# Kernel optimization log

Measured on AMD Instinct MI355X. Metric: run time of the kernel, lower is better.

Reference implementation:

```python
import jax, jax.numpy as jnp
import numpy as np

B, N, H = 1024, 4096, 32


def setup_inputs() -> dict:
    key = jax.random.key(0)
    ks = jax.random.split(key, 9)
    node_embedding = jax.random.normal(ks[0], (B, N, H), dtype=jnp.float32)
    mask = jax.random.randint(ks[1], (B, N), 0, 2).astype(jnp.float32)
    times = jax.random.uniform(ks[2], (B,), dtype=jnp.float32)
    idxc = jax.random.randint(ks[3], (B, 1), 0, N)
    # parameters
    vf = jax.random.uniform(ks[4], (1, H), dtype=jnp.float32)
    lim1 = 1.0 / np.sqrt(2 * H + 1)
    W1 = jax.random.uniform(ks[5], (H, 2 * H + 1), minval=-lim1, maxval=lim1, dtype=jnp.float32)
    b1 = jax.random.uniform(ks[6], (H,), minval=-lim1, maxval=lim1, dtype=jnp.float32)
    limh = 1.0 / np.sqrt(H)
    Wq = jax.random.uniform(ks[7], (H, H), minval=-limh, maxval=limh, dtype=jnp.float32)
    Wk = jax.random.uniform(ks[8], (H, H), minval=-limh, maxval=limh, dtype=jnp.float32)
    return {"node_embedding": node_embedding, "mask": mask, "times": times,
            "vf": vf, "W1": W1, "b1": b1, "Wq": Wq, "Wk": Wk, "idxc": idxc}


def reference(node_embedding, mask, times, vf, W1, b1, Wq, Wk, idxc):
    h = node_embedding.shape[-1]
    node_avg = jnp.mean(node_embedding, axis=1)                       # [B, H]
    # gather per-batch context node (idxc path; vf used only when idxc is None)
    f = jnp.take_along_axis(node_embedding, idxc[:, :, None], axis=1)[:, 0, :]  # [B, H]
    cat = jnp.concatenate([node_avg, f, times[:, None]], axis=1)      # [B, 2H+1]
    emb = cat @ W1.T + b1                                             # [B, H]
    q = emb @ Wq.T                                                    # [B, H]
    k = node_embedding @ Wk.T                                         # [B, N, H]
    scores = jnp.einsum('bh,bnh->bn', q, k) / jnp.sqrt(jnp.asarray(h, emb.dtype))
    scores = scores - mask * 999999999.0
    return jax.nn.softmax(scores, axis=-1)
```

## Files before the change

### kernel.cpp

```cpp
#include <hip/hip_runtime.h>
#include <math.h>

#define BB 1024
#define NN 4096
#define HH 32
#define PP 4
#define RK1 (NN / PP)

typedef float floatx4 __attribute__((ext_vector_type(4)));

#define WS_PART 0

__global__ __launch_bounds__(256) void k1_colsum(
    const float* __restrict__ ne, float* __restrict__ ws)
{
    const int blk = blockIdx.x;
    const int b   = blk >> 2;
    const int p   = blk & (PP - 1);
    const int tid = threadIdx.x;
    const int q8  = tid & 7;
    const int r   = tid >> 3;

    __shared__ float s_part[256 * 4];

    const float* base = ne + (size_t)b * (NN * HH)
                           + (size_t)(p * RK1 + r) * HH + q8 * 4;
    float a0 = 0.f, a1 = 0.f, a2 = 0.f, a3 = 0.f;
    #pragma unroll 8
    for (int i = 0; i < RK1 / 32; ++i) {
        const floatx4 v = __builtin_nontemporal_load(
            reinterpret_cast<const floatx4*>(base + i * (32 * HH)));
        a0 += v.x; a1 += v.y; a2 += v.z; a3 += v.w;
    }
    *reinterpret_cast<float4*>(&s_part[tid * 4]) = make_float4(a0, a1, a2, a3);
    __syncthreads();

    if (tid < HH) {
        const int q = tid >> 2, j = tid & 3;
        float s = 0.f;
        #pragma unroll
        for (int rr = 0; rr < 32; ++rr) s += s_part[(rr * 8 + q) * 4 + j];
        ws[WS_PART + (b * PP + p) * HH + tid] = s;
    }
}

__global__ __launch_bounds__(256) void k3_scores(
    const float* __restrict__ ne, const float* __restrict__ mask,
    const float* __restrict__ times,
    const float* __restrict__ W1, const float* __restrict__ b1,
    const float* __restrict__ Wq, const float* __restrict__ Wk,
    const int* __restrict__ idxc,
    const float* __restrict__ ws, float* __restrict__ out)
{
    const int b   = blockIdx.x;
    const int tid = threadIdx.x;
    const int q8  = tid & 7;
    const int r   = tid >> 3;

    __shared__ float s_scores[NN];
    __shared__ float sh_avg[HH], sh_f[HH], sh_emb[HH], sh_qk[HH];
    __shared__ float red_buf[4];

    if (tid < HH) {
        float s = 0.f;
        #pragma unroll
        for (int p = 0; p < PP; ++p) s += ws[WS_PART + (b * PP + p) * HH + tid];
        sh_avg[tid] = s * (1.0f / (float)NN);
        sh_f[tid]   = ne[(size_t)b * (NN * HH) + (size_t)idxc[b] * HH + tid];
    }
    __syncthreads();
    if (tid < HH) {
        const float t = times[b];
        const float* w = W1 + tid * (2 * HH + 1);
        float e = b1[tid];
        #pragma unroll
        for (int j = 0; j < HH; ++j) e += sh_avg[j] * w[j];
        #pragma unroll
        for (int j = 0; j < HH; ++j) e += sh_f[j] * w[HH + j];
        e += t * w[2 * HH];
        sh_emb[tid] = e;
    }
    __syncthreads();
    if (tid < HH) {
        const float* w = Wq + tid * HH;
        float qv = 0.f;
        #pragma unroll
        for (int j = 0; j < HH; ++j) qv += sh_emb[j] * w[j];
        sh_f[tid] = qv;
    }
    __syncthreads();
    if (tid < HH) {
        float s = 0.f;
        #pragma unroll
        for (int h = 0; h < HH; ++h) s += sh_f[h] * Wk[h * HH + tid];
        sh_qk[tid] = s * 0.17677669529663687f;
    }
    __syncthreads();

    const float kq0 = sh_qk[q8 * 4 + 0];
    const float kq1 = sh_qk[q8 * 4 + 1];
    const float kq2 = sh_qk[q8 * 4 + 2];
    const float kq3 = sh_qk[q8 * 4 + 3];

    const float* base = ne + (size_t)b * (NN * HH) + (size_t)r * HH + q8 * 4;

    #pragma unroll 8
    for (int i = 0; i < NN / 32; ++i) {
        const floatx4 v = __builtin_nontemporal_load(
            reinterpret_cast<const floatx4*>(base + i * (32 * HH)));
        float p = v.x * kq0 + v.y * kq1 + v.z * kq2 + v.w * kq3;
        p += __shfl_xor(p, 1);
        p += __shfl_xor(p, 2);
        p += __shfl_xor(p, 4);
        if (q8 == 0) s_scores[r + i * 32] = p;
    }
    __syncthreads();

    const float* mrow = mask + (size_t)b * NN;
    float lmax = -INFINITY;
    #pragma unroll
    for (int k = 0; k < NN / 1024; ++k) {
        const int n4 = tid + k * 256;
        const floatx4 mv = __builtin_nontemporal_load(
            reinterpret_cast<const floatx4*>(mrow + n4 * 4));
        float4 sv = *reinterpret_cast<const float4*>(&s_scores[n4 * 4]);
        sv.x -= mv.x * 999999999.0f;
        sv.y -= mv.y * 999999999.0f;
        sv.z -= mv.z * 999999999.0f;
        sv.w -= mv.w * 999999999.0f;
        *reinterpret_cast<float4*>(&s_scores[n4 * 4]) = sv;
        lmax = fmaxf(lmax, fmaxf(fmaxf(sv.x, sv.y), fmaxf(sv.z, sv.w)));
    }
    #pragma unroll
    for (int m = 1; m < 64; m <<= 1) lmax = fmaxf(lmax, __shfl_xor(lmax, m));
    if ((tid & 63) == 0) red_buf[tid >> 6] = lmax;
    __syncthreads();
    const float bmax = fmaxf(fmaxf(red_buf[0], red_buf[1]),
                             fmaxf(red_buf[2], red_buf[3]));

    float lsum = 0.f;
    #pragma unroll
    for (int k = 0; k < NN / 256; ++k) {
        const int n = tid + k * 256;
        const float e = expf(s_scores[n] - bmax);
        s_scores[n] = e;
        lsum += e;
    }
    #pragma unroll
    for (int m = 1; m < 64; m <<= 1) lsum += __shfl_xor(lsum, m);
    __syncthreads();
    if ((tid & 63) == 0) red_buf[tid >> 6] = lsum;
    __syncthreads();
    const float inv = 1.0f / (red_buf[0] + red_buf[1] + red_buf[2] + red_buf[3]);

    float* orow = out + (size_t)b * NN;
    #pragma unroll
    for (int k = 0; k < NN / 1024; ++k) {
        const int n4 = tid + k * 256;
        const float4 ev = *reinterpret_cast<const float4*>(&s_scores[n4 * 4]);
        floatx4 sv;
        sv.x = ev.x * inv; sv.y = ev.y * inv; sv.z = ev.z * inv; sv.w = ev.w * inv;
        __builtin_nontemporal_store(
            sv, reinterpret_cast<floatx4*>(orow + n4 * 4));
    }
}

extern "C" void kernel_launch(void* const* d_in, const int* in_sizes, int n_in,
                              void* d_out, int out_size, void* d_ws, size_t ws_size,
                              hipStream_t stream) {
    (void)in_sizes; (void)n_in; (void)ws_size; (void)out_size;
    const float* ne    = (const float*)d_in[0];
    const float* mask  = (const float*)d_in[1];
    const float* times = (const float*)d_in[2];
    const float* W1    = (const float*)d_in[4];
    const float* b1    = (const float*)d_in[5];
    const float* Wq    = (const float*)d_in[6];
    const float* Wk    = (const float*)d_in[7];
    const int*   idxc  = (const int*)d_in[8];
    float* out = (float*)d_out;
    float* ws  = (float*)d_ws;

    k1_colsum<<<dim3(BB * PP), dim3(256), 0, stream>>>(ne, ws);
    k3_scores<<<dim3(BB), dim3(256), 0, stream>>>(
        ne, mask, times, W1, b1, Wq, Wk, idxc, ws, out);
}
```

Measured before the change: 183.7 us.

## Fuse column-sum and score kernels into one cooperative grid-synced kernel

Replaces the two-kernel sequence with a single cooperative kernel of 2048 blocks. Each block first computes a half-row column sum, then a grid-wide sync runs, and half the blocks go on to compute the scores and softmax. This removes one kernel launch and the gap between kernels. In exchange it adds a grid barrier, leaves half the blocks idle in the second phase, and falls back to the old path if the cooperative launch fails.

```diff
diff --git a/kernel.cpp b/kernel.cpp
--- a/kernel.cpp
+++ b/kernel.cpp
@@ -1,15 +1,174 @@
 #include <hip/hip_runtime.h>
+#include <hip/hip_cooperative_groups.h>
 #include <math.h>
+
+namespace cg = cooperative_groups;
 
 #define BB 1024
 #define NN 4096
 #define HH 32
+#define GB 2048
+#define HR (NN / 2)
 #define PP 4
 #define RK1 (NN / PP)
 
 typedef float floatx4 __attribute__((ext_vector_type(4)));
 
 #define WS_PART 0
+#define WS_FB   (BB * 2 * HH)
+
+__global__ __launch_bounds__(256, 8) void fused(
+    const float* __restrict__ ne, const float* __restrict__ mask,
+    const float* __restrict__ times,
+    const float* __restrict__ W1, const float* __restrict__ b1,
+    const float* __restrict__ Wq, const float* __restrict__ Wk,
+    const int* __restrict__ idxc,
+    float* __restrict__ ws, float* __restrict__ out)
+{
+    __shared__ float smem[NN + 160];
+    const int tid = threadIdx.x;
+    const int g   = blockIdx.x;
+    const int q8  = tid & 7;
+    const int r   = tid >> 3;
+
+    {
+        const int b = g >> 1;
+        const int h = g & 1;
+        const float* base = ne + (size_t)b * (NN * HH)
+                               + (size_t)(h * HR + r) * HH + q8 * 4;
+        float a0 = 0.f, a1 = 0.f, a2 = 0.f, a3 = 0.f;
+        #pragma unroll 8
+        for (int i = 0; i < HR / 32; ++i) {
+            const floatx4 v = __builtin_nontemporal_load(
+                reinterpret_cast<const floatx4*>(base + i * (32 * HH)));
+            a0 += v.x; a1 += v.y; a2 += v.z; a3 += v.w;
+        }
+        *reinterpret_cast<float4*>(&smem[tid * 4]) = make_float4(a0, a1, a2, a3);
+        __syncthreads();
+
+        if (tid < HH) {
+            const int q = tid >> 2, j = tid & 3;
+            float s = 0.f;
+            #pragma unroll
+            for (int rr = 0; rr < 32; ++rr) s += smem[(rr * 8 + q) * 4 + j];
+            ws[WS_PART + (b * 2 + h) * HH + tid] = s;
+        }
+    }
+
+    cg::this_grid().sync();
+
+    if (g >= BB) return;
+    const int b = g;
+
+    float* s_scores = smem;
+    float* sh_avg   = smem + NN;
+    float* sh_f     = smem + NN + 32;
+    float* sh_emb   = smem + NN + 64;
+    float* sh_qk    = smem + NN + 96;
+    float* red_buf  = smem + NN + 128;
+
+    if (tid < HH) {
+        const float s = ws[WS_PART + (b * 2 + 0) * HH + tid]
+                      + ws[WS_PART + (b * 2 + 1) * HH + tid];
+        sh_avg[tid] = s * (1.0f / (float)NN);
+        sh_f[tid]   = ne[(size_t)b * (NN * HH) + (size_t)idxc[b] * HH + tid];
+    }
+    __syncthreads();
+    if (tid < HH) {
+        const float t = times[b];
+        const float* w = W1 + tid * (2 * HH + 1);
+        float e = b1[tid];
+        #pragma unroll
+        for (int j = 0; j < HH; ++j) e += sh_avg[j] * w[j];
+        #pragma unroll
+        for (int j = 0; j < HH; ++j) e += sh_f[j] * w[HH + j];
+        e += t * w[2 * HH];
+        sh_emb[tid] = e;
+    }
+    __syncthreads();
+    if (tid < HH) {
+        const float* w = Wq + tid * HH;
+        float qv = 0.f;
+        #pragma unroll
+        for (int j = 0; j < HH; ++j) qv += sh_emb[j] * w[j];
+        sh_f[tid] = qv;
+    }
+    __syncthreads();
+    if (tid < HH) {
+        float s = 0.f;
+        #pragma unroll
+        for (int h = 0; h < HH; ++h) s += sh_f[h] * Wk[h * HH + tid];
+        sh_qk[tid] = s * 0.17677669529663687f;
+    }
+    __syncthreads();
+
+    const float kq0 = sh_qk[q8 * 4 + 0];
+    const float kq1 = sh_qk[q8 * 4 + 1];
+    const float kq2 = sh_qk[q8 * 4 + 2];
+    const float kq3 = sh_qk[q8 * 4 + 3];
+
+    const float* base = ne + (size_t)b * (NN * HH) + (size_t)r * HH + q8 * 4;
+
+    #pragma unroll 8
+    for (int i = 0; i < NN / 32; ++i) {
+        const floatx4 v = __builtin_nontemporal_load(
+            reinterpret_cast<const floatx4*>(base + i * (32 * HH)));
+        float p = v.x * kq0 + v.y * kq1 + v.z * kq2 + v.w * kq3;
+        p += __shfl_xor(p, 1);
+        p += __shfl_xor(p, 2);
+        p += __shfl_xor(p, 4);
+        if (q8 == 0) s_scores[r + i * 32] = p;
+    }
+    __syncthreads();
+
+    const float* mrow = mask + (size_t)b * NN;
+    float lmax = -INFINITY;
+    #pragma unroll
+    for (int k = 0; k < NN / 1024; ++k) {
+        const int n4 = tid + k * 256;
+        const floatx4 mv = __builtin_nontemporal_load(
+            reinterpret_cast<const floatx4*>(mrow + n4 * 4));
+        float4 sv = *reinterpret_cast<const float4*>(&s_scores[n4 * 4]);
+        sv.x -= mv.x * 999999999.0f;
+        sv.y -= mv.y * 999999999.0f;
+        sv.z -= mv.z * 999999999.0f;
+        sv.w -= mv.w * 999999999.0f;
+        *reinterpret_cast<float4*>(&s_scores[n4 * 4]) = sv;
+        lmax = fmaxf(lmax, fmaxf(fmaxf(sv.x, sv.y), fmaxf(sv.z, sv.w)));
+    }
+    #pragma unroll
+    for (int m = 1; m < 64; m <<= 1) lmax = fmaxf(lmax, __shfl_xor(lmax, m));
+    if ((tid & 63) == 0) red_buf[tid >> 6] = lmax;
+    __syncthreads();
+    const float bmax = fmaxf(fmaxf(red_buf[0], red_buf[1]),
+                             fmaxf(red_buf[2], red_buf[3]));
+
+    float lsum = 0.f;
+    #pragma unroll
+    for (int k = 0; k < NN / 256; ++k) {
+        const int n = tid + k * 256;
+        const float e = expf(s_scores[n] - bmax);
+        s_scores[n] = e;
+        lsum += e;
+    }
+    #pragma unroll
+    for (int m = 1; m < 64; m <<= 1) lsum += __shfl_xor(lsum, m);
+    __syncthreads();
+    if ((tid & 63) == 0) red_buf[tid >> 6] = lsum;
+    __syncthreads();
+    const float inv = 1.0f / (red_buf[0] + red_buf[1] + red_buf[2] + red_buf[3]);
+
+    float* orow = out + (size_t)b * NN;
+    #pragma unroll
+    for (int k = 0; k < NN / 1024; ++k) {
+        const int n4 = tid + k * 256;
+        const float4 ev = *reinterpret_cast<const float4*>(&s_scores[n4 * 4]);
+        floatx4 sv;
+        sv.x = ev.x * inv; sv.y = ev.y * inv; sv.z = ev.z * inv; sv.w = ev.w * inv;
+        __builtin_nontemporal_store(
+            sv, reinterpret_cast<floatx4*>(orow + n4 * 4));
+    }
+}
 
 __global__ __launch_bounds__(256) void k1_colsum(
     const float* __restrict__ ne, float* __restrict__ ws)
@@ -40,7 +199,7 @@
         float s = 0.f;
         #pragma unroll
         for (int rr = 0; rr < 32; ++rr) s += s_part[(rr * 8 + q) * 4 + j];
-        ws[WS_PART + (b * PP + p) * HH + tid] = s;
+        ws[WS_FB + (b * PP + p) * HH + tid] = s;
     }
 }
 
@@ -64,7 +223,7 @@
     if (tid < HH) {
         float s = 0.f;
         #pragma unroll
-        for (int p = 0; p < PP; ++p) s += ws[WS_PART + (b * PP + p) * HH + tid];
+        for (int p = 0; p < PP; ++p) s += ws[WS_FB + (b * PP + p) * HH + tid];
         sh_avg[tid] = s * (1.0f / (float)NN);
         sh_f[tid]   = ne[(size_t)b * (NN * HH) + (size_t)idxc[b] * HH + tid];
     }
@@ -180,7 +339,14 @@
     float* out = (float*)d_out;
     float* ws  = (float*)d_ws;
 
-    k1_colsum<<<dim3(BB * PP), dim3(256), 0, stream>>>(ne, ws);
-    k3_scores<<<dim3(BB), dim3(256), 0, stream>>>(
-        ne, mask, times, W1, b1, Wq, Wk, idxc, ws, out);
+    void* args[] = {(void*)&ne, (void*)&mask, (void*)&times, (void*)&W1,
+                    (void*)&b1, (void*)&Wq, (void*)&Wk, (void*)&idxc,
+                    (void*)&ws, (void*)&out};
+    const hipError_t err = hipLaunchCooperativeKernel(
+        (const void*)fused, dim3(GB), dim3(256), args, 0, stream);
+    if (err != hipSuccess) {
+        k1_colsum<<<dim3(BB * PP), dim3(256), 0, stream>>>(ne, ws);
+        k3_scores<<<dim3(BB), dim3(256), 0, stream>>>(
+            ne, mask, times, W1, b1, Wq, Wk, idxc, ws, out);
+    }
 }
```

Result: slower. 449.2 us (+144.6%).
